# Performance work log

Measured on AMD Instinct MI355X. Metric: run time of the kernel, lower is better.

Reference implementation:

```python
import jax, jax.numpy as jnp
import numpy as np

T, B, E, H = 512, 128, 512, 512
MEM, CTX = 500, 300

def setup_inputs() -> dict:
    key = jax.random.key(0)
    ks = jax.random.split(key, 16)
    s = 0.05
    return {
        "input_seqs": jax.random.normal(ks[0], (B, T, E), jnp.float32),
        "input_lengths": jax.random.randint(ks[1], (B,), 1, T + 1),
        "Wih_f": jax.random.normal(ks[2], (4 * H, E + CTX), jnp.float32) * s,
        "Whh_f": jax.random.normal(ks[3], (4 * H, H), jnp.float32) * s,
        "bih_f": jax.random.normal(ks[4], (4 * H,), jnp.float32) * s,
        "bhh_f": jax.random.normal(ks[5], (4 * H,), jnp.float32) * s,
        "Wih_b": jax.random.normal(ks[6], (4 * H, E + CTX), jnp.float32) * s,
        "Whh_b": jax.random.normal(ks[7], (4 * H, H), jnp.float32) * s,
        "bih_b": jax.random.normal(ks[8], (4 * H,), jnp.float32) * s,
        "bhh_b": jax.random.normal(ks[9], (4 * H,), jnp.float32) * s,
        "Mk_f": jax.random.normal(ks[10], (MEM, H), jnp.float32) * s,
        "Mv_f": jax.random.normal(ks[11], (CTX, MEM), jnp.float32) * s,
        "Mk_b": jax.random.normal(ks[12], (MEM, H), jnp.float32) * s,
        "Mv_b": jax.random.normal(ks[13], (CTX, MEM), jnp.float32) * s,
    }

def _mem_ctx(h, Mk, Mv):
    # exp-key softmax read: exp(h Mk^T) normalized by row sum, then project to CTX
    a = jnp.exp(h @ Mk.T)                      # [B, MEM]
    return (a / jnp.sum(a, axis=-1, keepdims=True)) @ Mv.T  # [B, CTX]

def _cell(x, h, c, Wih, Whh, b):
    g = x @ Wih.T + h @ Whh.T + b              # [B, 4H], gate order i,f,g,o
    i, f, gg, o = jnp.split(g, 4, axis=-1)
    c = jax.nn.sigmoid(f) * c + jax.nn.sigmoid(i) * jnp.tanh(gg)
    return jax.nn.sigmoid(o) * jnp.tanh(c), c

def reference(input_seqs, input_lengths, Wih_f, Whh_f, bih_f, bhh_f,
              Wih_b, Whh_b, bih_b, bhh_b, Mk_f, Mv_f, Mk_b, Mv_b):
    xs = jnp.transpose(input_seqs, (1, 0, 2))          # [T, B, E]
    dt = xs.dtype
    mask = (jnp.arange(T)[:, None] < input_lengths[None, :]).astype(dt)[:, :, None]  # [T,B,1]
    b_f = bih_f + bhh_f
    b_b = bih_b + bhh_b
    z = jnp.zeros((B, H), dt)
    zf = jnp.zeros((), dt)
    one = jnp.ones((), dt)

    def fstep(carry, x):
        h, c, flag = carry
        ctx = flag * _mem_ctx(h, Mk_f, Mv_f)           # step 0 uses zero dummy context
        h, c = _cell(jnp.concatenate([x, ctx], -1), h, c, Wih_f, Whh_f, b_f)
        return (h, c, one), h
    _, f_hs = jax.lax.scan(fstep, (z, z, zf), xs)      # [T, B, H] per-step hidden

    def bstep(carry, xm):
        x, m = xm
        hm, h, c, flag = carry
        ctx = flag * _mem_ctx(hm, Mk_b, Mv_b)
        h, c = _cell(jnp.concatenate([x, ctx], -1), h, c, Wih_b, Whh_b, b_b)
        return (h * m, h, c, one), None                # masked hidden feeds next memory read
    (h_b, _, _, _), _ = jax.lax.scan(bstep, (z, z, z, zf), (xs[::-1], mask[::-1]))

    idx = jnp.clip(input_lengths - 1, 0, T - 1)
    h_f = f_hs[idx, jnp.arange(B)]                     # final valid forward hidden per example
    # permute(1,2,0).view(B,-1): interleave fwd/bwd per hidden unit
    return jnp.stack([h_f, h_b], axis=-1).reshape(B, 2 * H)
```

## Files before the change

kernel.cpp:

```cpp
#include <hip/hip_runtime.h>
#include <hip/hip_bf16.h>

#define T_   512
#define B_   128
#define E_   512
#define H_   512
#define G4_  2048
#define MEM_ 500
#define CTX_ 300
#define EC_  (E_ + CTX_)
#define SPIN_MAX 65536

typedef short sh8  __attribute__((ext_vector_type(8)));
typedef float f32x4 __attribute__((ext_vector_type(4)));

struct ScanParams {
  const float* __restrict__ x;
  const short* __restrict__ xbf;
  const int*   __restrict__ len;
  const float* __restrict__ Wih0; const float* __restrict__ Whh0;
  const float* __restrict__ bih0; const float* __restrict__ bhh0;
  const float* __restrict__ Wih1; const float* __restrict__ Whh1;
  const float* __restrict__ bih1; const float* __restrict__ bhh1;
  const float* __restrict__ Mk0;  const float* __restrict__ Mk1;
  const float* __restrict__ Mf;
  short* __restrict__ hbf;
  short* __restrict__ hmbf;
  short* __restrict__ aB;
  unsigned* __restrict__ bar;
  float* __restrict__ out;
};

__device__ __forceinline__ float sigm_(float x) { return 1.f / (1.f + __expf(-x)); }
__device__ __forceinline__ float tanh_(float x) { return 1.f - 2.f / (__expf(2.f * x) + 1.f); }
__device__ __forceinline__ short f2bs(float f) {
  __hip_bfloat16 h = __float2bfloat16(f);
  short s; __builtin_memcpy(&s, &h, 2); return s;
}
__device__ __forceinline__ float bs2f(short s) {
  unsigned u = ((unsigned)(unsigned short)s) << 16;
  float f; __builtin_memcpy(&f, &u, 4); return f;
}

struct F16 { sh8 v[16]; };
__device__ __forceinline__ void gld16(F16& f, const short* base) {
  asm volatile(
      "global_load_dwordx4 %0, %16, off sc0 sc1\n\t"
      "global_load_dwordx4 %1, %16, off offset:64 sc0 sc1\n\t"
      "global_load_dwordx4 %2, %16, off offset:128 sc0 sc1\n\t"
      "global_load_dwordx4 %3, %16, off offset:192 sc0 sc1\n\t"
      "global_load_dwordx4 %4, %16, off offset:256 sc0 sc1\n\t"
      "global_load_dwordx4 %5, %16, off offset:320 sc0 sc1\n\t"
      "global_load_dwordx4 %6, %16, off offset:384 sc0 sc1\n\t"
      "global_load_dwordx4 %7, %16, off offset:448 sc0 sc1\n\t"
      "global_load_dwordx4 %8, %16, off offset:512 sc0 sc1\n\t"
      "global_load_dwordx4 %9, %16, off offset:576 sc0 sc1\n\t"
      "global_load_dwordx4 %10, %16, off offset:640 sc0 sc1\n\t"
      "global_load_dwordx4 %11, %16, off offset:704 sc0 sc1\n\t"
      "global_load_dwordx4 %12, %16, off offset:768 sc0 sc1\n\t"
      "global_load_dwordx4 %13, %16, off offset:832 sc0 sc1\n\t"
      "global_load_dwordx4 %14, %16, off offset:896 sc0 sc1\n\t"
      "global_load_dwordx4 %15, %16, off offset:960 sc0 sc1\n\t"
      "s_waitcnt vmcnt(0)"
      : "=&v"(f.v[0]), "=&v"(f.v[1]), "=&v"(f.v[2]), "=&v"(f.v[3]),
        "=&v"(f.v[4]), "=&v"(f.v[5]), "=&v"(f.v[6]), "=&v"(f.v[7]),
        "=&v"(f.v[8]), "=&v"(f.v[9]), "=&v"(f.v[10]), "=&v"(f.v[11]),
        "=&v"(f.v[12]), "=&v"(f.v[13]), "=&v"(f.v[14]), "=&v"(f.v[15])
      : "v"(base)
      : "memory");
}

__device__ __forceinline__ void st4s(short* base, unsigned d0, unsigned d1,
                                     unsigned d2, unsigned d3) {
  asm volatile(
      "global_store_short %4, %0, off sc0 sc1\n\t"
      "global_store_short %4, %1, off offset:1024 sc0 sc1\n\t"
      "global_store_short %4, %2, off offset:2048 sc0 sc1\n\t"
      "global_store_short %4, %3, off offset:3072 sc0 sc1\n\t"
      "s_waitcnt vmcnt(0)"
      :: "v"(d0), "v"(d1), "v"(d2), "v"(d3), "v"(base) : "memory");
}

__device__ __forceinline__ void st8s(short* base, const unsigned* d) {
  asm volatile(
      "global_store_short %8, %0, off sc0 sc1\n\t"
      "global_store_short %8, %1, off offset:1024 sc0 sc1\n\t"
      "global_store_short %8, %2, off offset:2048 sc0 sc1\n\t"
      "global_store_short %8, %3, off offset:3072 sc0 sc1\n\t"
      "global_store_short %8, %4, off offset:8 sc0 sc1\n\t"
      "global_store_short %8, %5, off offset:1032 sc0 sc1\n\t"
      "global_store_short %8, %6, off offset:2056 sc0 sc1\n\t"
      "global_store_short %8, %7, off offset:3080 sc0 sc1"
      :: "v"(d[0]), "v"(d[1]), "v"(d[2]), "v"(d[3]),
         "v"(d[4]), "v"(d[5]), "v"(d[6]), "v"(d[7]), "v"(base) : "memory");
}

__device__ __forceinline__ bool hchk(const unsigned* hfl, int wv, unsigned ep, int lane) {
  unsigned v = __hip_atomic_load(&hfl[((lane * 8) + wv) * 16],
                                 __ATOMIC_RELAXED, __HIP_MEMORY_SCOPE_AGENT);
  return __all((int)(v >= ep));
}
__device__ __forceinline__ bool achk(const unsigned* afl, int wv, unsigned ep, int lane) {
  unsigned v = __hip_atomic_load(&afl[(((lane & 31) * 8) + wv) * 16],
                                 __ATOMIC_RELAXED, __HIP_MEMORY_SCOPE_AGENT);
  return __all((int)(v >= ep));
}
__device__ __forceinline__ void spin_h(const unsigned* hfl, int wv, unsigned ep, int lane) {
  int n = 0;
  while (!hchk(hfl, wv, ep, lane) && n < SPIN_MAX) { __builtin_amdgcn_s_sleep(1); ++n; }
}
__device__ __forceinline__ void spin_a(const unsigned* afl, int wv, unsigned ep, int lane) {
  int n = 0;
  while (!achk(afl, wv, ep, lane) && n < SPIN_MAX) { __builtin_amdgcn_s_sleep(1); ++n; }
}
__device__ __forceinline__ void fset(unsigned* slot, unsigned ep, int lane) {
  if (lane == 0)
    __hip_atomic_store(slot, ep, __ATOMIC_RELAXED, __HIP_MEMORY_SCOPE_AGENT);
}

__global__ __launch_bounds__(256) void xcvt_kernel(const float* __restrict__ x,
                                                   short* __restrict__ xbf) {
  const size_t i = ((size_t)blockIdx.x * 256 + threadIdx.x) * 8;
  f32x4 a = *reinterpret_cast<const f32x4*>(x + i);
  f32x4 b = *reinterpret_cast<const f32x4*>(x + i + 4);
  sh8 v;
  #pragma unroll
  for (int j = 0; j < 4; ++j) { v[j] = f2bs(a[j]); v[4 + j] = f2bs(b[j]); }
  *reinterpret_cast<sh8*>(xbf + i) = v;
}

__global__ __launch_bounds__(256) void mfused_kernel(
    const float* __restrict__ WihF, const float* __restrict__ WihB,
    const float* __restrict__ MvF,  const float* __restrict__ MvB,
    float* __restrict__ Mf) {
  const int d  = blockIdx.x >> 7;
  const int j0 = (blockIdx.x & 127) * 16;
  const float* __restrict__ Wih = d ? WihB : WihF;
  const float* __restrict__ Mv  = d ? MvB  : MvF;
  __shared__ float Wl[16][CTX_ + 1];
  for (int i = threadIdx.x; i < 16 * CTX_; i += 256) {
    int r = i / CTX_, cc = i - r * CTX_;
    Wl[r][cc] = Wih[(size_t)(j0 + r) * EC_ + E_ + cc];
  }
  __syncthreads();
  const int jj = threadIdx.x & 15;
  for (int m = threadIdx.x >> 4; m < MEM_; m += 16) {
    float acc = 0.f;
    for (int cc = 0; cc < CTX_; ++cc)
      acc = fmaf(Mv[cc * MEM_ + m], Wl[jj][cc], acc);
    Mf[(size_t)d * MEM_ * G4_ + (size_t)m * G4_ + j0 + jj] = acc;
  }
}

__global__ __launch_bounds__(512, 1) void scan_kernel(ScanParams p) {
  const int dir  = blockIdx.x >> 6;
  const int w    = blockIdx.x & 63;
  const int tid  = threadIdx.x;
  const int wv   = tid >> 6;
  const int lane = tid & 63;

  __shared__ __align__(16) short WgL[32 * 2 * 64 * 8];
  __shared__ __align__(16) short MkL[16 * 64 * 8];
  __shared__ __align__(16) short MfL[16 * 2 * 64 * 8];
  __shared__ int LvL[B_];

  const float* __restrict__ Wihd = dir ? p.Wih1 : p.Wih0;
  const float* __restrict__ Whhd = dir ? p.Whh1 : p.Whh0;
  const float* __restrict__ bihd = dir ? p.bih1 : p.bih0;
  const float* __restrict__ bhhd = dir ? p.bhh1 : p.bhh0;
  const float* __restrict__ Mkd  = dir ? p.Mk1  : p.Mk0;
  const float* __restrict__ Mfd  = p.Mf + (size_t)dir * MEM_ * G4_;
  short* __restrict__ aBd = p.aB + (size_t)dir * B_ * 512;

  unsigned* __restrict__ hflD = p.bar + (size_t)dir * 64 * 8 * 16;
  unsigned* __restrict__ aflD = p.bar + 16384 + (size_t)dir * 32 * 8 * 16;

  const bool prod = ((w & 1) == dir);
  const int  ct   = w >> 1;

  for (int i = tid; i < 32 * 2 * 64; i += 512) {
    const int ks = i >> 7, r2 = i & 127, ct2 = r2 >> 6, l2 = r2 & 63;
    const int col = l2 & 15, kg = l2 >> 4;
    const int k0 = ks * 32 + kg * 8;
    const int gc = (col & 3) * H_ + 8 * w + 4 * ct2 + (col >> 2);
    const float* src = (k0 < E_) ? (Wihd + (size_t)gc * EC_ + k0)
                                 : (Whhd + (size_t)gc * H_ + (k0 - E_));
    sh8 v;
    #pragma unroll
    for (int j = 0; j < 8; ++j) v[j] = f2bs(src[j]);
    *reinterpret_cast<sh8*>(&WgL[i * 8]) = v;
  }
  for (int i = tid; i < 16 * 64; i += 512) {
    const int ks = i >> 6, l2 = i & 63;
    const int col = l2 & 15, kg = l2 >> 4;
    const int k0 = ks * 32 + kg * 8;
    const int mr = 16 * ct + col;
    sh8 v;
    #pragma unroll
    for (int j = 0; j < 8; ++j)
      v[j] = (mr < MEM_) ? f2bs(Mkd[(size_t)mr * H_ + k0 + j]) : (short)0;
    *reinterpret_cast<sh8*>(&MkL[i * 8]) = v;
  }
  for (int i = tid; i < 16 * 2 * 64; i += 512) {
    const int ks = i >> 7, r2 = i & 127, ct2 = r2 >> 6, l2 = r2 & 63;
    const int col = l2 & 15, kg = l2 >> 4;
    const int gc = (col & 3) * H_ + 8 * w + 4 * ct2 + (col >> 2);
    const int m0 = ks * 32 + kg * 8;
    sh8 v;
    #pragma unroll
    for (int j = 0; j < 8; ++j)
      v[j] = (m0 + j < MEM_) ? f2bs(Mfd[(size_t)(m0 + j) * G4_ + gc]) : (short)0;
    *reinterpret_cast<sh8*>(&MfL[i * 8]) = v;
  }
  if (tid < B_) LvL[tid] = p.len[tid];

  const int cc  = lane & 15;
  const int q   = cc & 3;
  const int uu  = cc >> 2;
  const int kg8 = (lane >> 4) * 8;
  const int arow = lane & 15;
  float biasl[2];
  #pragma unroll
  for (int ct2 = 0; ct2 < 2; ++ct2) {
    const int gc = q * H_ + 8 * w + 4 * ct2 + uu;
    biasl[ct2] = bihd[gc] + bhhd[gc];
  }

  float creg[2][4] = {{0.f,0.f,0.f,0.f},{0.f,0.f,0.f,0.f}};
  __syncthreads();

  auto xhalf = [&](int t, f32x4* acc) {
    if (p.xbf) {
      const short* xb = p.xbf + ((size_t)(16 * wv + arow) * T_ + t) * E_ + kg8;
      for (int ks = 0; ks < 16; ++ks) {
        sh8 af = *reinterpret_cast<const sh8*>(xb + ks * 32);
        acc[0] = __builtin_amdgcn_mfma_f32_16x16x32_bf16(
            af, *reinterpret_cast<const sh8*>(&WgL[((ks * 2 + 0) * 64 + lane) * 8]), acc[0], 0, 0, 0);
        acc[1] = __builtin_amdgcn_mfma_f32_16x16x32_bf16(
            af, *reinterpret_cast<const sh8*>(&WgL[((ks * 2 + 1) * 64 + lane) * 8]), acc[1], 0, 0, 0);
      }
    } else {
      const float* xp0 = p.x + ((size_t)(16 * wv + arow) * T_ + t) * E_ + kg8;
      for (int ks = 0; ks < 16; ++ks) {
        f32x4 v0 = *reinterpret_cast<const f32x4*>(xp0 + ks * 32);
        f32x4 v1 = *reinterpret_cast<const f32x4*>(xp0 + ks * 32 + 4);
        sh8 af;
        #pragma unroll
        for (int j = 0; j < 4; ++j) { af[j] = f2bs(v0[j]); af[4 + j] = f2bs(v1[j]); }
        acc[0] = __builtin_amdgcn_mfma_f32_16x16x32_bf16(
            af, *reinterpret_cast<const sh8*>(&WgL[((ks * 2 + 0) * 64 + lane) * 8]), acc[0], 0, 0, 0);
        acc[1] = __builtin_amdgcn_mfma_f32_16x16x32_bf16(
            af, *reinterpret_cast<const sh8*>(&WgL[((ks * 2 + 1) * 64 + lane) * 8]), acc[1], 0, 0, 0);
      }
    }
  };

  f32x4 accG[2] = {(f32x4){0,0,0,0}, (f32x4){0,0,0,0}};
  xhalf(dir ? T_ - 1 : 0, accG);

  const bool bwdprod = prod && dir;

  for (int s = 0; s < T_; ++s) {
    const int t   = dir ? (T_ - 1 - s) : s;
    const int cur = s & 1, prv = cur ^ 1;
    const short* __restrict__ hb_prev = p.hbf + ((size_t)(prv * 2 + dir)) * B_ * H_;
    short*       __restrict__ hb_cur  = p.hbf + ((size_t)(cur * 2 + dir)) * B_ * H_;
    const short* __restrict__ hm_prev = p.hmbf + (size_t)prv * B_ * H_;
    short*       __restrict__ hm_cur  = p.hmbf + (size_t)cur * B_ * H_;

    const short* hrow = hb_prev + (size_t)(16 * wv + arow) * H_ + kg8;
    const short* mrow = hm_prev + (size_t)(16 * wv + arow) * H_ + kg8;

    if (s > 0) spin_h(hflD, wv, (unsigned)s, lane);
    __builtin_amdgcn_sched_barrier(0);
    F16 fH, fM;
    gld16(fH, hrow);
    if (bwdprod) gld16(fM, mrow);

    if (prod) {
      f32x4 accA = (f32x4){0, 0, 0, 0};
      if (dir) {
        for (int ks = 0; ks < 16; ++ks)
          accA = __builtin_amdgcn_mfma_f32_16x16x32_bf16(
              fM.v[ks], *reinterpret_cast<const sh8*>(&MkL[(ks * 64 + lane) * 8]), accA, 0, 0, 0);
      } else {
        for (int ks = 0; ks < 16; ++ks)
          accA = __builtin_amdgcn_mfma_f32_16x16x32_bf16(
              fH.v[ks], *reinterpret_cast<const sh8*>(&MkL[(ks * 64 + lane) * 8]), accA, 0, 0, 0);
      }
      const int m = 16 * ct + arow;
      unsigned d[4];
      #pragma unroll
      for (int r = 0; r < 4; ++r) {
        float e = (m < MEM_) ? __expf(accA[r]) : 0.f;
        d[r] = (unsigned)(unsigned short)f2bs(e);
      }
      st4s(aBd + (size_t)(16 * wv + 4 * (lane >> 4)) * 512 + m, d[0], d[1], d[2], d[3]);
      fset(&aflD[(ct * 8 + wv) * 16], (unsigned)(s + 1), lane);
    }

    for (int ks = 0; ks < 16; ++ks) {
      accG[0] = __builtin_amdgcn_mfma_f32_16x16x32_bf16(
          fH.v[ks], *reinterpret_cast<const sh8*>(&WgL[(((16 + ks) * 2 + 0) * 64 + lane) * 8]), accG[0], 0, 0, 0);
      accG[1] = __builtin_amdgcn_mfma_f32_16x16x32_bf16(
          fH.v[ks], *reinterpret_cast<const sh8*>(&WgL[(((16 + ks) * 2 + 1) * 64 + lane) * 8]), accG[1], 0, 0, 0);
    }

    f32x4 accC[2] = {(f32x4){0,0,0,0}, (f32x4){0,0,0,0}};
    float inv4[4] = {0.f, 0.f, 0.f, 0.f};
    if (s > 0) {
      spin_a(aflD, wv, (unsigned)(s + 1), lane);
      __builtin_amdgcn_sched_barrier(0);
      F16 fC;
      gld16(fC, aBd + (size_t)(16 * wv + arow) * 512 + kg8);
      float rs = 0.f;
      for (int ks = 0; ks < 16; ++ks) {
        accC[0] = __builtin_amdgcn_mfma_f32_16x16x32_bf16(
            fC.v[ks], *reinterpret_cast<const sh8*>(&MfL[((ks * 2 + 0) * 64 + lane) * 8]), accC[0], 0, 0, 0);
        accC[1] = __builtin_amdgcn_mfma_f32_16x16x32_bf16(
            fC.v[ks], *reinterpret_cast<const sh8*>(&MfL[((ks * 2 + 1) * 64 + lane) * 8]), accC[1], 0, 0, 0);
        #pragma unroll
        for (int j = 0; j < 8; ++j) rs += bs2f(fC.v[ks][j]);
      }
      rs += __shfl_xor(rs, 16);
      rs += __shfl_xor(rs, 32);
      #pragma unroll
      for (int r = 0; r < 4; ++r)
        inv4[r] = 1.f / __shfl(rs, 4 * (lane >> 4) + r);
    }

    unsigned hsd[8]; unsigned hmd[8]; float hvv[2][4];
    #pragma unroll
    for (int ct2 = 0; ct2 < 2; ++ct2) {
      float g4[4];
      #pragma unroll
      for (int r = 0; r < 4; ++r) {
        float v = accG[ct2][r] + biasl[ct2];
        if (s > 0) v += accC[ct2][r] * inv4[r];
        g4[r] = v;
      }
      #pragma unroll
      for (int r = 0; r < 4; ++r) {
        const float x1 = __shfl_xor(g4[r], 1);
        const float x2 = __shfl_xor(g4[r], 2);
        const float x3 = __shfl_xor(g4[r], 3);
        const float iv = (q==0)?g4[r]:(q==1)?x1:(q==2)?x2:x3;
        const float fv = (q==0)?x1:(q==1)?g4[r]:(q==2)?x3:x2;
        const float gv = (q==0)?x2:(q==1)?x3:(q==2)?g4[r]:x1;
        const float ov = (q==0)?x3:(q==1)?x2:(q==2)?x1:g4[r];
        float cv = creg[ct2][r];
        cv = sigm_(fv) * cv + sigm_(iv) * tanh_(gv);
        const float hv = sigm_(ov) * tanh_(cv);
        creg[ct2][r] = cv;
        hvv[ct2][r] = hv;
        const short hs = f2bs(hv);
        hsd[ct2 * 4 + r] = (unsigned)(unsigned short)hs;
        if (dir) {
          const int b = 16 * wv + 4 * (lane >> 4) + r;
          hmd[ct2 * 4 + r] = (t < LvL[b]) ? hsd[ct2 * 4 + r] : 0u;
        }
      }
    }
    if (q == 0) {
      const int b0 = 16 * wv + 4 * (lane >> 4);
      const int unit0 = 8 * w + uu;
      unsigned hord[8] = {hsd[0],hsd[1],hsd[2],hsd[3],hsd[4],hsd[5],hsd[6],hsd[7]};
      st8s(hb_cur + (size_t)b0 * H_ + unit0, hord);
      if (dir) {
        unsigned mord[8] = {hmd[0],hmd[1],hmd[2],hmd[3],hmd[4],hmd[5],hmd[6],hmd[7]};
        st8s(hm_cur + (size_t)b0 * H_ + unit0, mord);
      }
      #pragma unroll
      for (int ct2 = 0; ct2 < 2; ++ct2) {
        #pragma unroll
        for (int r = 0; r < 4; ++r) {
          const int b = b0 + r;
          const int unit = unit0 + 4 * ct2;
          if (dir == 0) {
            if (t == LvL[b] - 1) p.out[b * (2 * H_) + 2 * unit] = hvv[ct2][r];
          } else {
            if (s == T_ - 1) p.out[b * (2 * H_) + 2 * unit + 1] = hvv[ct2][r];
          }
        }
      }
    }
    asm volatile("s_waitcnt vmcnt(0)" ::: "memory");
    fset(&hflD[(w * 8 + wv) * 16], (unsigned)(s + 1), lane);

    accG[0] = (f32x4){0,0,0,0}; accG[1] = (f32x4){0,0,0,0};
    if (s + 1 < T_) xhalf(dir ? (T_ - 2 - s) : (s + 1), accG);
  }
}

extern "C" void kernel_launch(void* const* d_in, const int* in_sizes, int n_in,
                              void* d_out, int out_size, void* d_ws, size_t ws_size,
                              hipStream_t stream) {
  (void)in_sizes; (void)n_in; (void)out_size;

  ScanParams p;
  p.x    = (const float*)d_in[0];
  p.len  = (const int*)  d_in[1];
  p.Wih0 = (const float*)d_in[2];
  p.Whh0 = (const float*)d_in[3];
  p.bih0 = (const float*)d_in[4];
  p.bhh0 = (const float*)d_in[5];
  p.Wih1 = (const float*)d_in[6];
  p.Whh1 = (const float*)d_in[7];
  p.bih1 = (const float*)d_in[8];
  p.bhh1 = (const float*)d_in[9];
  p.Mk0  = (const float*)d_in[10];
  const float* MvF = (const float*)d_in[11];
  p.Mk1  = (const float*)d_in[12];
  const float* MvB = (const float*)d_in[13];

  char* ws = (char*)d_ws;
  size_t off = 0;
  auto alloc = [&](size_t bytes) -> void* {
    void* ptr = ws + off; off += (bytes + 255) & ~(size_t)255; return ptr;
  };
  float*    Mf   = (float*)   alloc((size_t)2 * MEM_ * G4_ * 4);
  short*    hbf  = (short*)   alloc((size_t)2 * 2 * B_ * H_ * 2);
  short*    hmbf = (short*)   alloc((size_t)2 * B_ * H_ * 2);
  short*    aB   = (short*)   alloc((size_t)2 * B_ * 512 * 2);
  unsigned* bar  = (unsigned*)alloc((size_t)24576 * sizeof(unsigned));
  size_t xbf_off = off;
  short*    xbf  = (short*)   alloc((size_t)B_ * T_ * E_ * 2);
  const bool useXbf = (ws_size >= xbf_off + (size_t)B_ * T_ * E_ * 2);

  p.Mf = Mf; p.hbf = hbf; p.hmbf = hmbf; p.aB = aB; p.bar = bar;
  p.xbf = useXbf ? xbf : nullptr;
  p.out = (float*)d_out;

  hipMemsetAsync(hbf, 0, (size_t)(2 * 2 + 2) * B_ * H_ * 2, stream);
  hipMemsetAsync(bar, 0, (size_t)24576 * sizeof(unsigned), stream);

  if (useXbf) {
    const size_t n8 = (size_t)B_ * T_ * E_ / 8;
    xcvt_kernel<<<dim3((unsigned)(n8 / 256)), dim3(256), 0, stream>>>(p.x, xbf);
  }
  mfused_kernel<<<dim3(256), dim3(256), 0, stream>>>(
      (const float*)d_in[2], (const float*)d_in[6], MvF, MvB, Mf);

  void* args[] = { &p };
  hipLaunchCooperativeKernel((const void*)scan_kernel, dim3(128), dim3(512),
                             args, 0, stream);
}
```

Measured before the change: 9.677 ms.

## Pack flags contiguously, stage stores through LDS, overlap next-step x projection

Replaces the padded, strided per-wave flag arrays with compact contiguous rows, so each spin poll reads one contiguous line per wave instead of scattered cache lines. The scattered 2-byte stores of hidden states and attention weights are staged through shared memory and written as 16-byte vector stores. The next timestep's input projection now runs right after the recurrent MMA and before the attention wait, so it overlaps the cross-block synchronisation latency. The cost is an extra LDS round trip and possible false sharing between packed flags.

```diff
diff --git a/kernel.cpp b/kernel.cpp
--- a/kernel.cpp
+++ b/kernel.cpp
@@ -70,48 +70,26 @@
       : "memory");
 }
 
-__device__ __forceinline__ void st4s(short* base, unsigned d0, unsigned d1,
-                                     unsigned d2, unsigned d3) {
-  asm volatile(
-      "global_store_short %4, %0, off sc0 sc1\n\t"
-      "global_store_short %4, %1, off offset:1024 sc0 sc1\n\t"
-      "global_store_short %4, %2, off offset:2048 sc0 sc1\n\t"
-      "global_store_short %4, %3, off offset:3072 sc0 sc1\n\t"
-      "s_waitcnt vmcnt(0)"
-      :: "v"(d0), "v"(d1), "v"(d2), "v"(d3), "v"(base) : "memory");
-}
-
-__device__ __forceinline__ void st8s(short* base, const unsigned* d) {
-  asm volatile(
-      "global_store_short %8, %0, off sc0 sc1\n\t"
-      "global_store_short %8, %1, off offset:1024 sc0 sc1\n\t"
-      "global_store_short %8, %2, off offset:2048 sc0 sc1\n\t"
-      "global_store_short %8, %3, off offset:3072 sc0 sc1\n\t"
-      "global_store_short %8, %4, off offset:8 sc0 sc1\n\t"
-      "global_store_short %8, %5, off offset:1032 sc0 sc1\n\t"
-      "global_store_short %8, %6, off offset:2056 sc0 sc1\n\t"
-      "global_store_short %8, %7, off offset:3080 sc0 sc1"
-      :: "v"(d[0]), "v"(d[1]), "v"(d[2]), "v"(d[3]),
-         "v"(d[4]), "v"(d[5]), "v"(d[6]), "v"(d[7]), "v"(base) : "memory");
-}
-
-__device__ __forceinline__ bool hchk(const unsigned* hfl, int wv, unsigned ep, int lane) {
-  unsigned v = __hip_atomic_load(&hfl[((lane * 8) + wv) * 16],
-                                 __ATOMIC_RELAXED, __HIP_MEMORY_SCOPE_AGENT);
+__device__ __forceinline__ void st16(short* addr, sh8 v) {
+  asm volatile("global_store_dwordx4 %0, %1, off sc0 sc1"
+               :: "v"(addr), "v"(v) : "memory");
+}
+
+__device__ __forceinline__ bool hchk(const unsigned* hrow, unsigned ep, int lane) {
+  unsigned v = __hip_atomic_load(&hrow[lane], __ATOMIC_RELAXED, __HIP_MEMORY_SCOPE_AGENT);
   return __all((int)(v >= ep));
 }
-__device__ __forceinline__ bool achk(const unsigned* afl, int wv, unsigned ep, int lane) {
-  unsigned v = __hip_atomic_load(&afl[(((lane & 31) * 8) + wv) * 16],
-                                 __ATOMIC_RELAXED, __HIP_MEMORY_SCOPE_AGENT);
+__device__ __forceinline__ bool achk(const unsigned* arow, unsigned ep, int lane) {
+  unsigned v = __hip_atomic_load(&arow[lane & 31], __ATOMIC_RELAXED, __HIP_MEMORY_SCOPE_AGENT);
   return __all((int)(v >= ep));
 }
-__device__ __forceinline__ void spin_h(const unsigned* hfl, int wv, unsigned ep, int lane) {
+__device__ __forceinline__ void spin_h(const unsigned* hrow, unsigned ep, int lane) {
   int n = 0;
-  while (!hchk(hfl, wv, ep, lane) && n < SPIN_MAX) { __builtin_amdgcn_s_sleep(1); ++n; }
-}
-__device__ __forceinline__ void spin_a(const unsigned* afl, int wv, unsigned ep, int lane) {
+  while (!hchk(hrow, ep, lane) && n < SPIN_MAX) { __builtin_amdgcn_s_sleep(1); ++n; }
+}
+__device__ __forceinline__ void spin_a(const unsigned* arow, unsigned ep, int lane) {
   int n = 0;
-  while (!achk(afl, wv, ep, lane) && n < SPIN_MAX) { __builtin_amdgcn_s_sleep(1); ++n; }
+  while (!achk(arow, ep, lane) && n < SPIN_MAX) { __builtin_amdgcn_s_sleep(1); ++n; }
 }
 __device__ __forceinline__ void fset(unsigned* slot, unsigned ep, int lane) {
   if (lane == 0)
@@ -162,6 +140,8 @@
   __shared__ __align__(16) short WgL[32 * 2 * 64 * 8];
   __shared__ __align__(16) short MkL[16 * 64 * 8];
   __shared__ __align__(16) short MfL[16 * 2 * 64 * 8];
+  __shared__ __align__(16) short HsL[8][16][8];
+  __shared__ __align__(16) short AsL[8][16][16];
   __shared__ int LvL[B_];
 
   const float* __restrict__ Wihd = dir ? p.Wih1 : p.Wih0;
@@ -172,8 +152,8 @@
   const float* __restrict__ Mfd  = p.Mf + (size_t)dir * MEM_ * G4_;
   short* __restrict__ aBd = p.aB + (size_t)dir * B_ * 512;
 
-  unsigned* __restrict__ hflD = p.bar + (size_t)dir * 64 * 8 * 16;
-  unsigned* __restrict__ aflD = p.bar + 16384 + (size_t)dir * 32 * 8 * 16;
+  unsigned* __restrict__ hrow_fl = p.bar + (size_t)(dir * 8 + wv) * 64;
+  unsigned* __restrict__ arow_fl = p.bar + 1024 + (size_t)(dir * 8 + wv) * 32;
 
   const bool prod = ((w & 1) == dir);
   const int  ct   = w >> 1;
@@ -219,6 +199,7 @@
   const int uu  = cc >> 2;
   const int kg8 = (lane >> 4) * 8;
   const int arow = lane & 15;
+  const int rg   = lane >> 4;
   float biasl[2];
   #pragma unroll
   for (int ct2 = 0; ct2 < 2; ++ct2) {
@@ -255,8 +236,8 @@
     }
   };
 
-  f32x4 accG[2] = {(f32x4){0,0,0,0}, (f32x4){0,0,0,0}};
-  xhalf(dir ? T_ - 1 : 0, accG);
+  f32x4 accX[2] = {(f32x4){0,0,0,0}, (f32x4){0,0,0,0}};
+  xhalf(dir ? T_ - 1 : 0, accX);
 
   const bool bwdprod = prod && dir;
 
@@ -271,7 +252,9 @@
     const short* hrow = hb_prev + (size_t)(16 * wv + arow) * H_ + kg8;
     const short* mrow = hm_prev + (size_t)(16 * wv + arow) * H_ + kg8;
 
-    if (s > 0) spin_h(hflD, wv, (unsigned)s, lane);
+    f32x4 accG[2] = { accX[0], accX[1] };
+
+    if (s > 0) spin_h(hrow_fl, (unsigned)s, lane);
     __builtin_amdgcn_sched_barrier(0);
     F16 fH, fM;
     gld16(fH, hrow);
@@ -289,14 +272,20 @@
               fH.v[ks], *reinterpret_cast<const sh8*>(&MkL[(ks * 64 + lane) * 8]), accA, 0, 0, 0);
       }
       const int m = 16 * ct + arow;
-      unsigned d[4];
       #pragma unroll
       for (int r = 0; r < 4; ++r) {
         float e = (m < MEM_) ? __expf(accA[r]) : 0.f;
-        d[r] = (unsigned)(unsigned short)f2bs(e);
-      }
-      st4s(aBd + (size_t)(16 * wv + 4 * (lane >> 4)) * 512 + m, d[0], d[1], d[2], d[3]);
-      fset(&aflD[(ct * 8 + wv) * 16], (unsigned)(s + 1), lane);
+        AsL[wv][4 * rg + r][arow] = f2bs(e);
+      }
+      asm volatile("s_waitcnt lgkmcnt(0)" ::: "memory");
+      __builtin_amdgcn_sched_barrier(0);
+      if (lane < 32) {
+        const int row = lane >> 1, half = lane & 1;
+        sh8 v = *reinterpret_cast<const sh8*>(&AsL[wv][row][half * 8]);
+        st16(aBd + (size_t)(16 * wv + row) * 512 + 16 * ct + 8 * half, v);
+      }
+      asm volatile("s_waitcnt vmcnt(0)" ::: "memory");
+      fset(&arow_fl[ct], (unsigned)(s + 1), lane);
     }
 
     for (int ks = 0; ks < 16; ++ks) {
@@ -306,10 +295,13 @@
           fH.v[ks], *reinterpret_cast<const sh8*>(&WgL[(((16 + ks) * 2 + 1) * 64 + lane) * 8]), accG[1], 0, 0, 0);
     }
 
+    accX[0] = (f32x4){0,0,0,0}; accX[1] = (f32x4){0,0,0,0};
+    if (s + 1 < T_) xhalf(dir ? (T_ - 2 - s) : (s + 1), accX);
+
     f32x4 accC[2] = {(f32x4){0,0,0,0}, (f32x4){0,0,0,0}};
     float inv4[4] = {0.f, 0.f, 0.f, 0.f};
     if (s > 0) {
-      spin_a(aflD, wv, (unsigned)(s + 1), lane);
+      spin_a(arow_fl, (unsigned)(s + 1), lane);
       __builtin_amdgcn_sched_barrier(0);
       F16 fC;
       gld16(fC, aBd + (size_t)(16 * wv + arow) * 512 + kg8);
@@ -329,7 +321,7 @@
         inv4[r] = 1.f / __shfl(rs, 4 * (lane >> 4) + r);
     }
 
-    unsigned hsd[8]; unsigned hmd[8]; float hvv[2][4];
+    unsigned hsd[8]; float hvv[2][4];
     #pragma unroll
     for (int ct2 = 0; ct2 < 2; ++ct2) {
       float g4[4];
@@ -353,23 +345,31 @@
         const float hv = sigm_(ov) * tanh_(cv);
         creg[ct2][r] = cv;
         hvv[ct2][r] = hv;
-        const short hs = f2bs(hv);
-        hsd[ct2 * 4 + r] = (unsigned)(unsigned short)hs;
-        if (dir) {
-          const int b = 16 * wv + 4 * (lane >> 4) + r;
-          hmd[ct2 * 4 + r] = (t < LvL[b]) ? hsd[ct2 * 4 + r] : 0u;
-        }
+        hsd[ct2 * 4 + r] = (unsigned)(unsigned short)f2bs(hv);
       }
     }
     if (q == 0) {
-      const int b0 = 16 * wv + 4 * (lane >> 4);
+      #pragma unroll
+      for (int ct2 = 0; ct2 < 2; ++ct2)
+        #pragma unroll
+        for (int r = 0; r < 4; ++r)
+          HsL[wv][4 * rg + r][4 * ct2 + uu] = (short)hsd[ct2 * 4 + r];
+    }
+    asm volatile("s_waitcnt lgkmcnt(0)" ::: "memory");
+    __builtin_amdgcn_sched_barrier(0);
+    if (lane < 16) {
+      const int row = lane;
+      sh8 hv8 = *reinterpret_cast<const sh8*>(&HsL[wv][row][0]);
+      st16(hb_cur + (size_t)(16 * wv + row) * H_ + 8 * w, hv8);
+      if (dir) {
+        sh8 zz = (sh8){0,0,0,0,0,0,0,0};
+        const bool keep = (t < LvL[16 * wv + row]);
+        st16(hm_cur + (size_t)(16 * wv + row) * H_ + 8 * w, keep ? hv8 : zz);
+      }
+    }
+    if (q == 0) {
+      const int b0 = 16 * wv + 4 * rg;
       const int unit0 = 8 * w + uu;
-      unsigned hord[8] = {hsd[0],hsd[1],hsd[2],hsd[3],hsd[4],hsd[5],hsd[6],hsd[7]};
-      st8s(hb_cur + (size_t)b0 * H_ + unit0, hord);
-      if (dir) {
-        unsigned mord[8] = {hmd[0],hmd[1],hmd[2],hmd[3],hmd[4],hmd[5],hmd[6],hmd[7]};
-        st8s(hm_cur + (size_t)b0 * H_ + unit0, mord);
-      }
       #pragma unroll
       for (int ct2 = 0; ct2 < 2; ++ct2) {
         #pragma unroll
@@ -385,10 +385,7 @@
       }
     }
     asm volatile("s_waitcnt vmcnt(0)" ::: "memory");
-    fset(&hflD[(w * 8 + wv) * 16], (unsigned)(s + 1), lane);
-
-    accG[0] = (f32x4){0,0,0,0}; accG[1] = (f32x4){0,0,0,0};
-    if (s + 1 < T_) xhalf(dir ? (T_ - 2 - s) : (s + 1), accG);
+    fset(&hrow_fl[w], (unsigned)(s + 1), lane);
   }
 }
 
@@ -422,7 +419,7 @@
   short*    hbf  = (short*)   alloc((size_t)2 * 2 * B_ * H_ * 2);
   short*    hmbf = (short*)   alloc((size_t)2 * B_ * H_ * 2);
   short*    aB   = (short*)   alloc((size_t)2 * B_ * 512 * 2);
-  unsigned* bar  = (unsigned*)alloc((size_t)24576 * sizeof(unsigned));
+  unsigned* bar  = (unsigned*)alloc((size_t)1536 * sizeof(unsigned));
   size_t xbf_off = off;
   short*    xbf  = (short*)   alloc((size_t)B_ * T_ * E_ * 2);
   const bool useXbf = (ws_size >= xbf_off + (size_t)B_ * T_ * E_ * 2);
@@ -432,7 +429,7 @@
   p.out = (float*)d_out;
 
   hipMemsetAsync(hbf, 0, (size_t)(2 * 2 + 2) * B_ * H_ * 2, stream);
-  hipMemsetAsync(bar, 0, (size_t)24576 * sizeof(unsigned), stream);
+  hipMemsetAsync(bar, 0, (size_t)1536 * sizeof(unsigned), stream);
 
   if (useXbf) {
     const size_t n8 = (size_t)B_ * T_ * E_ / 8;
```

Measured after the change: 11.04 ms. 14.1% more time.
